# Optimization experiments

Measured on AMD Instinct MI355X. Metric: run time of the kernel, lower is better.

The kernel has to match this reference:

```python
import jax, jax.numpy as jnp
import numpy as np

T, D, H, V, Z = 32, 128, 256, 32000, 256


def _gru_cell(x, h, W_ih, W_hh, b_ih, b_hh):
    # PyTorch GRU cell, gate order r,z,n. x,h: [D,H]
    gi = x @ W_ih.T + b_ih
    gh = h @ W_hh.T + b_hh
    i_r, i_z, i_n = jnp.split(gi, 3, axis=-1)
    h_r, h_z, h_n = jnp.split(gh, 3, axis=-1)
    r = jax.nn.sigmoid(i_r + h_r)
    z = jax.nn.sigmoid(i_z + h_z)
    n = jnp.tanh(i_n + r * h_n)
    return (1.0 - z) * n + z * h


def _tree_rnn(nodes, edges, h0, emb, pc, ps):
    # nodes/edges: [T,D]; h0: [D,H]. Child vs sibling GRU chosen per-node by edges.
    def step(h, te):
        tok, e = te
        x = emb[tok]                       # [D,H]
        hc = _gru_cell(x, h, *pc)
        hs = _gru_cell(x, h, *ps)
        hn = jnp.where(e[:, None], hc, hs)  # branch-aware state update
        return hn, hn                       # seq_len=1, L=1 => output == new state
    h_final, outs = jax.lax.scan(step, h0, (nodes, edges))
    return outs, h_final                    # outs: [T,D,H]


def setup_inputs() -> dict:
    key = jax.random.key(0)
    ks = iter(jax.random.split(key, 48))
    s = 0.05
    def gru():
        return (jax.random.normal(next(ks), (3 * H, H), jnp.float32) * s,
                jax.random.normal(next(ks), (3 * H, H), jnp.float32) * s,
                jnp.zeros((3 * H,), jnp.float32),
                jnp.zeros((3 * H,), jnp.float32))
    inp = {}
    inp['nodes'] = jax.random.randint(next(ks), (T, D), 0, V, dtype=jnp.int32)
    inp['edges'] = jax.random.bernoulli(next(ks), 0.5, (T, D))
    inp['emb'] = jax.random.normal(next(ks), (V, H), jnp.float32) * s
    (inp['enc_c_Wih'], inp['enc_c_Whh'], inp['enc_c_bih'], inp['enc_c_bhh']) = gru()
    (inp['enc_s_Wih'], inp['enc_s_Whh'], inp['enc_s_bih'], inp['enc_s_bhh']) = gru()
    (inp['dec_c_Wih'], inp['dec_c_Whh'], inp['dec_c_bih'], inp['dec_c_bhh']) = gru()
    (inp['dec_s_Wih'], inp['dec_s_Whh'], inp['dec_s_bih'], inp['dec_s_bhh']) = gru()
    inp['W_mean'] = jax.random.normal(next(ks), (Z, H), jnp.float32) * s
    inp['b_mean'] = jnp.zeros((Z,), jnp.float32)
    inp['W_logv'] = jax.random.normal(next(ks), (Z, H), jnp.float32) * s
    inp['b_logv'] = jnp.zeros((Z,), jnp.float32)
    inp['W_l2h'] = jax.random.normal(next(ks), (H, Z), jnp.float32) * s
    inp['b_l2h'] = jnp.zeros((H,), jnp.float32)
    inp['W_out'] = jax.random.normal(next(ks), (V, H), jnp.float32) * s
    inp['b_out'] = jnp.zeros((V,), jnp.float32)
    inp['enc_init'] = jax.random.normal(next(ks), (D, H), jnp.float32) * 0.001
    inp['eps'] = jax.random.normal(next(ks), (D, Z), jnp.float32)
    return inp


def reference(nodes, edges, emb,
              enc_c_Wih, enc_c_Whh, enc_c_bih, enc_c_bhh,
              enc_s_Wih, enc_s_Whh, enc_s_bih, enc_s_bhh,
              dec_c_Wih, dec_c_Whh, dec_c_bih, dec_c_bhh,
              dec_s_Wih, dec_s_Whh, dec_s_bih, dec_s_bhh,
              W_mean, b_mean, W_logv, b_logv, W_l2h, b_l2h,
              W_out, b_out, enc_init, eps):
    pc_e = (enc_c_Wih, enc_c_Whh, enc_c_bih, enc_c_bhh)
    ps_e = (enc_s_Wih, enc_s_Whh, enc_s_bih, enc_s_bhh)
    pc_d = (dec_c_Wih, dec_c_Whh, dec_c_bih, dec_c_bhh)
    ps_d = (dec_s_Wih, dec_s_Whh, dec_s_bih, dec_s_bhh)

    _, hid = _tree_rnn(nodes, edges, enc_init, emb, pc_e, ps_e)  # [D,H]
    mean = hid @ W_mean.T + b_mean                               # [D,Z]
    logv = hid @ W_logv.T + b_logv
    z = eps * jnp.exp(0.5 * logv) + mean                          # reparameterize
    h0 = z @ W_l2h.T + b_l2h                                      # [D,H]
    outs, _ = _tree_rnn(nodes, edges, h0, emb, pc_d, ps_d)        # [T,D,H]
    logits = outs @ W_out.T + b_out                               # [T,D,V]
    logp = jax.nn.log_softmax(logits, axis=-1)
    return logp, mean, logv, z
```

## Files before the change

kernel.cpp:

```cpp
#include <hip/hip_runtime.h>
#include <hip/hip_bf16.h>

#define TT 32
#define DD 128
#define HH 256
#define VV 32000
#define ZZ 256
#define NTL 50
#define NBLK 16
#define GHLP 100

typedef __attribute__((ext_vector_type(8))) short bf16x8;
typedef __attribute__((ext_vector_type(4))) float f32x4;
typedef __attribute__((ext_vector_type(8))) _Float16 f16x8;

static __device__ inline unsigned short f2bf(float x) {
    __hip_bfloat16 h = __float2bfloat16(x);
    return *(unsigned short*)&h;
}

static __device__ inline unsigned long long pack4h(_Float16 a, _Float16 b,
                                                   _Float16 c, _Float16 d) {
    union { _Float16 h[4]; unsigned long long u; } x;
    x.h[0] = a; x.h[1] = b; x.h[2] = c; x.h[3] = d;
    return x.u;
}

static __device__ inline void gload_lds16(const void* g, void* l) {
    __builtin_amdgcn_global_load_lds(
        (const __attribute__((address_space(1))) void*)g,
        (__attribute__((address_space(3))) void*)l, 16, 0, 0);
}

__global__ void edge_canon_k(const unsigned char* __restrict__ eb,
                             unsigned char* __restrict__ canon)
{
    __shared__ int flag;
    if (threadIdx.x == 0) flag = 0;
    __syncthreads();
    int acc = 0;
    for (int i = threadIdx.x; i < TT * DD; i += 256)
        if (i & 3) acc |= eb[i];
    if (acc) atomicOr(&flag, 1);
    __syncthreads();
    const bool is_i32 = (flag == 0);
    for (int i = threadIdx.x; i < TT * DD; i += 256)
        canon[i] = is_i32 ? eb[4 * (size_t)i] : eb[i];
}

__global__ __launch_bounds__(256) void pack_frag(
    const float* __restrict__ src, __hip_bfloat16* __restrict__ dst, int nchunks_total)
{
    int i = blockIdx.x * 256 + threadIdx.x;
    if (i >= nchunks_total) return;
    int lane = i & 63, ks = (i >> 6) & 7, j = i >> 9;
    int g = lane >> 4, c = lane & 15;
    const float* s = src + (size_t)(j * 16 + c) * HH + ks * 32 + g * 8;
    float4 v0 = *(const float4*)s;
    float4 v1 = *(const float4*)(s + 4);
    bf16x8 o;
    o[0] = (short)f2bf(v0.x); o[1] = (short)f2bf(v0.y);
    o[2] = (short)f2bf(v0.z); o[3] = (short)f2bf(v0.w);
    o[4] = (short)f2bf(v1.x); o[5] = (short)f2bf(v1.y);
    o[6] = (short)f2bf(v1.z); o[7] = (short)f2bf(v1.w);
    *(bf16x8*)(dst + (size_t)i * 8) = o;
}

__global__ __launch_bounds__(256) void pack_frag4(
    const float* __restrict__ s0, const float* __restrict__ s1,
    const float* __restrict__ s2, const float* __restrict__ s3,
    __hip_bfloat16* __restrict__ dst)
{
    int i = blockIdx.x * 256 + threadIdx.x;
    if (i >= 24576) return;
    int slot = blockIdx.y;
    const float* src = (slot == 0) ? s0 : (slot == 1) ? s1 : (slot == 2) ? s2 : s3;
    __hip_bfloat16* d = dst + (size_t)slot * 196608;
    int lane = i & 63, ks = (i >> 6) & 7, j = i >> 9;
    int g = lane >> 4, c = lane & 15;
    const float* s = src + (size_t)(j * 16 + c) * HH + ks * 32 + g * 8;
    float4 v0 = *(const float4*)s;
    float4 v1 = *(const float4*)(s + 4);
    bf16x8 o;
    o[0] = (short)f2bf(v0.x); o[1] = (short)f2bf(v0.y);
    o[2] = (short)f2bf(v0.z); o[3] = (short)f2bf(v0.w);
    o[4] = (short)f2bf(v1.x); o[5] = (short)f2bf(v1.y);
    o[6] = (short)f2bf(v1.z); o[7] = (short)f2bf(v1.w);
    *(bf16x8*)(d + (size_t)i * 8) = o;
}

__global__ __launch_bounds__(256) void pack_wrnn4(
    const float* __restrict__ s0, const float* __restrict__ s1,
    const float* __restrict__ s2, const float* __restrict__ s3,
    _Float16* __restrict__ dst)
{
    int i = blockIdx.x * 256 + threadIdx.x;
    if (i >= 24576) return;
    int slot = blockIdx.y;
    const float* src = (slot == 0) ? s0 : (slot == 1) ? s1 : (slot == 2) ? s2 : s3;
    _Float16* d = dst + (size_t)slot * 196608;
    int lane = i & 63;
    int t2 = i >> 6;
    int ks = t2 & 7;
    int t3 = t2 >> 3;
    int tt = t3 % 6;
    int j8 = t3 / 6;
    int g = lane >> 4, c = lane & 15;
    int jg2 = tt / 3, gt = tt % 3;
    int srow = gt * 256 + j8 * 32 + jg2 * 16 + c;
    int scol = ks * 32 + g * 8;
    const float* s = src + (size_t)srow * HH + scol;
    float4 v0 = *(const float4*)s;
    float4 v1 = *(const float4*)(s + 4);
    f16x8 o;
    o[0] = (_Float16)v0.x; o[1] = (_Float16)v0.y;
    o[2] = (_Float16)v0.z; o[3] = (_Float16)v0.w;
    o[4] = (_Float16)v1.x; o[5] = (_Float16)v1.y;
    o[6] = (_Float16)v1.z; o[7] = (_Float16)v1.w;
    *(f16x8*)(d + (size_t)i * 8) = o;
}

__global__ __launch_bounds__(256) void gather_pack(
    const int* __restrict__ nodes, const float* __restrict__ emb,
    __hip_bfloat16* __restrict__ dst)
{
    int i = blockIdx.x * 256 + threadIdx.x;
    int lane = i & 63, ks = (i >> 6) & 7, j = i >> 9;
    int g = lane >> 4, c = lane & 15;
    int row = j * 16 + c;
    int tok = nodes[row];
    const float* s = emb + (size_t)tok * HH + ks * 32 + g * 8;
    float4 v0 = *(const float4*)s;
    float4 v1 = *(const float4*)(s + 4);
    bf16x8 o;
    o[0] = (short)f2bf(v0.x); o[1] = (short)f2bf(v0.y);
    o[2] = (short)f2bf(v0.z); o[3] = (short)f2bf(v0.w);
    o[4] = (short)f2bf(v1.x); o[5] = (short)f2bf(v1.y);
    o[6] = (short)f2bf(v1.z); o[7] = (short)f2bf(v1.w);
    *(bf16x8*)(dst + (size_t)i * 8) = o;
}

__global__ __launch_bounds__(256) void pack_lat3(
    const float* __restrict__ s0, const float* __restrict__ s1,
    const float* __restrict__ s2, float* __restrict__ dst)
{
    int i = blockIdx.x * 256 + threadIdx.x;
    int slot = blockIdx.y;
    const float* src = (slot == 0) ? s0 : (slot == 1) ? s1 : s2;
    float* d = dst + (size_t)slot * 65536;
    int j = i & 255, k = i >> 8;
    d[(size_t)k * 256 + j] = src[(size_t)j * 256 + k];
}

template<int MT, bool WRITE_C, bool HAS_BIAS, bool LSE_PARTIAL, bool LSE_SUB>
__global__ __launch_bounds__(256, 2) void gemm_rs(
    const __hip_bfloat16* __restrict__ A,
    const __hip_bfloat16* __restrict__ B,
    int ldc, int nchunks, int ntiles,
    const float* __restrict__ bias,
    const float* __restrict__ lse,
    float* __restrict__ C,
    float* __restrict__ pm, float* __restrict__ ps)
{
    __shared__ float lds_st[WRITE_C ? (4 * 16 * 68) : 1];

    const int tid  = threadIdx.x;
    const int w    = tid >> 6;
    const int lane = tid & 63;
    const int g    = lane >> 4;
    const int c    = lane & 15;
    const int m0   = blockIdx.x * (64 * MT);
    const int n0   = blockIdx.y * (nchunks * 64);
    const int jb0  = n0 >> 4;

    bf16x8 a[MT][8];
#pragma unroll
    for (int mt = 0; mt < MT; ++mt) {
        const int row16 = m0 + mt * 64 + w * 16;
        const __hip_bfloat16* ap = A + (((size_t)(row16 >> 4) * 8) * 64 + lane) * 8;
#pragma unroll
        for (int ks = 0; ks < 8; ++ks) a[mt][ks] = *(const bf16x8*)(ap + ks * 512);
    }

    float mrun[MT][4], srun[MT][4];
#pragma unroll
    for (int mt = 0; mt < MT; ++mt)
#pragma unroll
        for (int r = 0; r < 4; ++r) { mrun[mt][r] = -3.0e38f; srun[mt][r] = 0.f; }

    float lsev[MT][4];
    if (LSE_SUB) {
#pragma unroll
        for (int mt = 0; mt < MT; ++mt)
#pragma unroll
            for (int r = 0; r < 4; ++r)
                lsev[mt][r] = lse[m0 + mt * 64 + w * 16 + 4 * g + r];
    }

    for (int nc = 0; nc < nchunks; ++nc) {
        const int nb = n0 + nc * 64;
        const __hip_bfloat16* bp = B + (((size_t)(jb0 + nc * 4) * 8) * 64 + lane) * 8;

        f32x4 acc[MT][4];
#pragma unroll
        for (int mt = 0; mt < MT; ++mt)
#pragma unroll
            for (int nf = 0; nf < 4; ++nf) acc[mt][nf] = (f32x4){0.f, 0.f, 0.f, 0.f};

#pragma unroll
        for (int ks = 0; ks < 8; ++ks) {
            bf16x8 b0 = *(const bf16x8*)(bp + (0 * 8 + ks) * 512);
            bf16x8 b1 = *(const bf16x8*)(bp + (1 * 8 + ks) * 512);
            bf16x8 b2 = *(const bf16x8*)(bp + (2 * 8 + ks) * 512);
            bf16x8 b3 = *(const bf16x8*)(bp + (3 * 8 + ks) * 512);
#pragma unroll
            for (int mt = 0; mt < MT; ++mt) {
                acc[mt][0] = __builtin_amdgcn_mfma_f32_16x16x32_bf16(a[mt][ks], b0, acc[mt][0], 0, 0, 0);
                acc[mt][1] = __builtin_amdgcn_mfma_f32_16x16x32_bf16(a[mt][ks], b1, acc[mt][1], 0, 0, 0);
                acc[mt][2] = __builtin_amdgcn_mfma_f32_16x16x32_bf16(a[mt][ks], b2, acc[mt][2], 0, 0, 0);
                acc[mt][3] = __builtin_amdgcn_mfma_f32_16x16x32_bf16(a[mt][ks], b3, acc[mt][3], 0, 0, 0);
            }
        }

        float bv[4] = {0.f, 0.f, 0.f, 0.f};
        if (HAS_BIAS) {
#pragma unroll
            for (int nf = 0; nf < 4; ++nf) bv[nf] = bias[nb + nf * 16 + c];
        }

        if (LSE_PARTIAL) {
#pragma unroll
            for (int mt = 0; mt < MT; ++mt)
#pragma unroll
                for (int r = 0; r < 4; ++r) {
                    float l0 = acc[mt][0][r] + bv[0];
                    float l1 = acc[mt][1][r] + bv[1];
                    float l2 = acc[mt][2][r] + bv[2];
                    float l3 = acc[mt][3][r] + bv[3];
                    float mc = fmaxf(fmaxf(l0, l1), fmaxf(l2, l3));
                    float mn = fmaxf(mrun[mt][r], mc);
                    srun[mt][r] = srun[mt][r] * __expf(mrun[mt][r] - mn)
                            + __expf(l0 - mn) + __expf(l1 - mn)
                            + __expf(l2 - mn) + __expf(l3 - mn);
                    mrun[mt][r] = mn;
                }
        }

        if (WRITE_C) {
            const int base = w * (16 * 68);
#pragma unroll
            for (int mt = 0; mt < MT; ++mt) {
                const int row16 = m0 + mt * 64 + w * 16;
#pragma unroll
                for (int nf = 0; nf < 4; ++nf)
#pragma unroll
                    for (int r = 0; r < 4; ++r) {
                        float v = acc[mt][nf][r] + bv[nf];
                        if (LSE_SUB) v -= lsev[mt][r];
                        lds_st[base + (4 * g + r) * 68 + nf * 16 + c] = v;
                    }
#pragma unroll
                for (int i = 0; i < 4; ++i) {
                    int lr = i * 4 + g;
                    float4 v = *(const float4*)&lds_st[base + lr * 68 + c * 4];
                    *(float4*)(C + (size_t)(row16 + lr) * ldc + nb + c * 4) = v;
                }
            }
        }
    }

    if (LSE_PARTIAL) {
#pragma unroll
        for (int mt = 0; mt < MT; ++mt)
#pragma unroll
            for (int r = 0; r < 4; ++r) {
                float m = mrun[mt][r], s = srun[mt][r];
#pragma unroll
                for (int mk = 1; mk <= 8; mk <<= 1) {
                    float m2 = __shfl_xor(m, mk);
                    float s2 = __shfl_xor(s, mk);
                    float mn = fmaxf(m, m2);
                    s = s * __expf(m - mn) + s2 * __expf(m2 - mn);
                    m = mn;
                }
                if (c == 0) {
                    int row = m0 + mt * 64 + w * 16 + 4 * g + r;
                    pm[(size_t)row * ntiles + blockIdx.y] = m;
                    ps[(size_t)row * ntiles + blockIdx.y] = s;
                }
            }
    }
}

template<bool WRITE_C, bool HAS_BIAS, bool LSE_PARTIAL, bool LSE_SUB>
__global__ __launch_bounds__(256, 2) void gemm_ls(
    const __hip_bfloat16* __restrict__ A,
    const __hip_bfloat16* __restrict__ B,
    int ldc, int nchunks, int ntiles,
    const float* __restrict__ bias,
    const float* __restrict__ lse,
    float* __restrict__ C,
    float* __restrict__ pm, float* __restrict__ ps)
{
    __shared__ __align__(16) char ldsB[2][32768];
    __shared__ float lds_st[WRITE_C ? (4 * 16 * 68) : 1];

    const int tid  = threadIdx.x;
    const int w    = tid >> 6;
    const int lane = tid & 63;
    const int g    = lane >> 4;
    const int c    = lane & 15;
    const int m0   = blockIdx.x * 128;
    const int n0   = blockIdx.y * (nchunks * 64);
    const int jb0  = n0 >> 4;

    bf16x8 a[2][8];
#pragma unroll
    for (int mt = 0; mt < 2; ++mt) {
        const int row16 = m0 + mt * 64 + w * 16;
        const __hip_bfloat16* ap = A + (((size_t)(row16 >> 4) * 8) * 64 + lane) * 8;
#pragma unroll
        for (int ks = 0; ks < 8; ++ks) a[mt][ks] = *(const bf16x8*)(ap + ks * 512);
    }

    float mrun[2][4], srun[2][4];
#pragma unroll
    for (int mt = 0; mt < 2; ++mt)
#pragma unroll
        for (int r = 0; r < 4; ++r) { mrun[mt][r] = -3.0e38f; srun[mt][r] = 0.f; }

    float lsev[2][4];
    if (LSE_SUB) {
#pragma unroll
        for (int mt = 0; mt < 2; ++mt)
#pragma unroll
            for (int r = 0; r < 4; ++r)
                lsev[mt][r] = lse[m0 + mt * 64 + w * 16 + 4 * g + r];
    }

    const char* Bbase = (const char*)B;
#define STAGE_TILE(bbuf, nc_)                                                     \
    {                                                                             \
        const char* src = Bbase + ((size_t)(jb0 + (nc_) * 4) * 8 * 64) * 16;      \
        _Pragma("unroll")                                                         \
        for (int i_ = 0; i_ < 8; ++i_) {                                          \
            int seg = w * 8 + i_;                                                 \
            gload_lds16(src + (size_t)seg * 1024 + lane * 16,                     \
                        &ldsB[bbuf][seg * 1024]);                                 \
        }                                                                         \
    }

    int buf = 0;
    STAGE_TILE(0, 0);
    __syncthreads();

    for (int nc = 0; nc < nchunks; ++nc) {
        if (nc + 1 < nchunks) STAGE_TILE(buf ^ 1, nc + 1);

        const int nb = n0 + nc * 64;
        f32x4 acc[2][4];
#pragma unroll
        for (int mt = 0; mt < 2; ++mt)
#pragma unroll
            for (int nf = 0; nf < 4; ++nf) acc[mt][nf] = (f32x4){0.f, 0.f, 0.f, 0.f};

#pragma unroll
        for (int ks = 0; ks < 8; ++ks) {
            bf16x8 b0 = *(const bf16x8*)&ldsB[buf][((0 * 8 + ks) * 64 + lane) * 16];
            bf16x8 b1 = *(const bf16x8*)&ldsB[buf][((1 * 8 + ks) * 64 + lane) * 16];
            bf16x8 b2 = *(const bf16x8*)&ldsB[buf][((2 * 8 + ks) * 64 + lane) * 16];
            bf16x8 b3 = *(const bf16x8*)&ldsB[buf][((3 * 8 + ks) * 64 + lane) * 16];
#pragma unroll
            for (int mt = 0; mt < 2; ++mt) {
                acc[mt][0] = __builtin_amdgcn_mfma_f32_16x16x32_bf16(a[mt][ks], b0, acc[mt][0], 0, 0, 0);
                acc[mt][1] = __builtin_amdgcn_mfma_f32_16x16x32_bf16(a[mt][ks], b1, acc[mt][1], 0, 0, 0);
                acc[mt][2] = __builtin_amdgcn_mfma_f32_16x16x32_bf16(a[mt][ks], b2, acc[mt][2], 0, 0, 0);
                acc[mt][3] = __builtin_amdgcn_mfma_f32_16x16x32_bf16(a[mt][ks], b3, acc[mt][3], 0, 0, 0);
            }
        }

        float bv[4] = {0.f, 0.f, 0.f, 0.f};
        if (HAS_BIAS) {
#pragma unroll
            for (int nf = 0; nf < 4; ++nf) bv[nf] = bias[nb + nf * 16 + c];
        }

        if (LSE_PARTIAL) {
#pragma unroll
            for (int mt = 0; mt < 2; ++mt)
#pragma unroll
                for (int r = 0; r < 4; ++r) {
                    float l0 = acc[mt][0][r] + bv[0];
                    float l1 = acc[mt][1][r] + bv[1];
                    float l2 = acc[mt][2][r] + bv[2];
                    float l3 = acc[mt][3][r] + bv[3];
                    float mc = fmaxf(fmaxf(l0, l1), fmaxf(l2, l3));
                    float mn = fmaxf(mrun[mt][r], mc);
                    srun[mt][r] = srun[mt][r] * __expf(mrun[mt][r] - mn)
                            + __expf(l0 - mn) + __expf(l1 - mn)
                            + __expf(l2 - mn) + __expf(l3 - mn);
                    mrun[mt][r] = mn;
                }
        }

        if (WRITE_C) {
            const int base = w * (16 * 68);
#pragma unroll
            for (int mt = 0; mt < 2; ++mt) {
                const int row16 = m0 + mt * 64 + w * 16;
#pragma unroll
                for (int nf = 0; nf < 4; ++nf)
#pragma unroll
                    for (int r = 0; r < 4; ++r) {
                        float v = acc[mt][nf][r] + bv[nf];
                        if (LSE_SUB) v -= lsev[mt][r];
                        lds_st[base + (4 * g + r) * 68 + nf * 16 + c] = v;
                    }
#pragma unroll
                for (int i = 0; i < 4; ++i) {
                    int lr = i * 4 + g;
                    float4 v = *(const float4*)&lds_st[base + lr * 68 + c * 4];
                    *(float4*)(C + (size_t)(row16 + lr) * ldc + nb + c * 4) = v;
                }
            }
        }

        __syncthreads();
        buf ^= 1;
    }
#undef STAGE_TILE

    if (LSE_PARTIAL) {
#pragma unroll
        for (int mt = 0; mt < 2; ++mt)
#pragma unroll
            for (int r = 0; r < 4; ++r) {
                float m = mrun[mt][r], s = srun[mt][r];
#pragma unroll
                for (int mk = 1; mk <= 8; mk <<= 1) {
                    float m2 = __shfl_xor(m, mk);
                    float s2 = __shfl_xor(s, mk);
                    float mn = fmaxf(m, m2);
                    s = s * __expf(m - mn) + s2 * __expf(m2 - mn);
                    m = mn;
                }
                if (c == 0) {
                    int row = m0 + mt * 64 + w * 16 + 4 * g + r;
                    pm[(size_t)row * ntiles + blockIdx.y] = m;
                    ps[(size_t)row * ntiles + blockIdx.y] = s;
                }
            }
    }
}

__global__ __launch_bounds__(512) void rnn_fused6(
    const unsigned char* __restrict__ ecan,
    const float* __restrict__ gi,
    const _Float16* __restrict__ Wr,
    const float* __restrict__ ecbih, const float* __restrict__ ecbhh,
    const float* __restrict__ esbih, const float* __restrict__ esbhh,
    const float* __restrict__ dcbih, const float* __restrict__ dcbhh,
    const float* __restrict__ dsbih, const float* __restrict__ dsbhh,
    const float* __restrict__ WmT, const float* __restrict__ WlT,
    const float* __restrict__ WhT,
    const float* __restrict__ b_mean, const float* __restrict__ b_logv,
    const float* __restrict__ b_l2h,
    const float* __restrict__ enc_init, const float* __restrict__ eps,
    float* __restrict__ out_mean, float* __restrict__ out_logv,
    float* __restrict__ out_z,
    __hip_bfloat16* __restrict__ outs_pk,
    _Float16* __restrict__ xh,
    int* __restrict__ flags)
{
    __shared__ _Float16 wlds[6 * 8 * 64 * 8];
    __shared__ _Float16 hpk[64 * 64 * 8];
    __shared__ _Float16 ghl[DD * GHLP];
    __shared__ float    bsum[4 * 256];
    __shared__ unsigned char ecan_l[TT * DD];

    const int v   = blockIdx.x & 1;
    const int j8  = blockIdx.x >> 1;
    const int tid = threadIdx.x;
    const int w    = tid >> 6;
    const int lane = tid & 63;
    const int g    = lane >> 4;
    const int c    = lane & 15;
    const int dq   = w & 3;
    const int jg2  = w >> 2;

    for (int u = tid; u < TT * DD; u += 512) ecan_l[u] = ecan[u];

    for (int u = tid; u < 4096; u += 512) {
        int chunk = u >> 6, ln = u & 63;
        int dt = chunk >> 3, ks = chunk & 7, lg = ln >> 4, lc = ln & 15;
        const float* s = enc_init + (size_t)(dt * 16 + lc) * HH + ks * 32 + lg * 8;
        float4 v0 = *(const float4*)s;
        float4 v1 = *(const float4*)(s + 4);
        f16x8 o;
        o[0] = (_Float16)v0.x; o[1] = (_Float16)v0.y;
        o[2] = (_Float16)v0.z; o[3] = (_Float16)v0.w;
        o[4] = (_Float16)v1.x; o[5] = (_Float16)v1.y;
        o[6] = (_Float16)v1.z; o[7] = (_Float16)v1.w;
        *(f16x8*)&hpk[(size_t)u * 8] = o;
    }
    __syncthreads();

    int bi = 0;

    for (int p = 0; p < 2; ++p) {
        {
            const _Float16* wsrc = Wr + ((size_t)(p * 2 + v) * 8 + j8) * (3072 * 8);
            for (int idx = tid; idx < 3072; idx += 512)
                *(f16x8*)&wlds[(size_t)idx * 8] = *(const f16x8*)(wsrc + (size_t)idx * 8);
        }
        {
            const float* bih = p ? (v ? dsbih : dcbih) : (v ? esbih : ecbih);
            const float* bhh = p ? (v ? dsbhh : dcbhh) : (v ? esbhh : ecbhh);
            if (tid < 256) {
                bsum[tid]       = bih[tid]       + bhh[tid];
                bsum[256 + tid] = bih[256 + tid] + bhh[256 + tid];
                bsum[512 + tid] = bih[512 + tid];
                bsum[768 + tid] = bhh[512 + tid];
            }
        }
        __syncthreads();

        for (int st = 0; st < TT; ++st) {
            f32x4 gpr0[3], gpr1[3];
            bool sel0, sel1;
            {
                const int u0 = tid, u1 = tid + 512;
                const int d0 = u0 >> 3, d1 = u1 >> 3;
                const int jgA = j8 * 32 + (u0 & 7) * 4;
                const int jgB = j8 * 32 + (u1 & 7) * 4;
                sel0 = (ecan_l[st * DD + d0] != 0) == (v == 0);
                sel1 = (ecan_l[st * DD + d1] != 0) == (v == 0);
                if (sel0) {
                    const float* gp = gi + (size_t)(st * DD + d0) * 3072 + p * 1536 + v * 768 + jgA;
                    gpr0[0] = *(const f32x4*)gp;
                    gpr0[1] = *(const f32x4*)(gp + 256);
                    gpr0[2] = *(const f32x4*)(gp + 512);
                }
                if (sel1) {
                    const float* gp = gi + (size_t)(st * DD + d1) * 3072 + p * 1536 + v * 768 + jgB;
                    gpr1[0] = *(const f32x4*)gp;
                    gpr1[1] = *(const f32x4*)(gp + 256);
                    gpr1[2] = *(const f32x4*)(gp + 512);
                }
            }

            f32x4 acc[2][3];
#pragma unroll
            for (int a = 0; a < 2; ++a)
#pragma unroll
                for (int b = 0; b < 3; ++b) acc[a][b] = (f32x4){0.f, 0.f, 0.f, 0.f};
#pragma unroll
            for (int ks = 0; ks < 8; ++ks) {
                f16x8 a0 = *(const f16x8*)&hpk[(((dq * 2 + 0) * 8 + ks) * 64 + lane) * 8];
                f16x8 a1 = *(const f16x8*)&hpk[(((dq * 2 + 1) * 8 + ks) * 64 + lane) * 8];
#pragma unroll
                for (int gt = 0; gt < 3; ++gt) {
                    f16x8 bf = *(const f16x8*)&wlds[(((jg2 * 3 + gt) * 8 + ks) * 64 + lane) * 8];
                    acc[0][gt] = __builtin_amdgcn_mfma_f32_16x16x32_f16(a0, bf, acc[0][gt], 0, 0, 0);
                    acc[1][gt] = __builtin_amdgcn_mfma_f32_16x16x32_f16(a1, bf, acc[1][gt], 0, 0, 0);
                }
            }

#pragma unroll
            for (int dti = 0; dti < 2; ++dti) {
                const int dt = dq * 2 + dti;
#pragma unroll
                for (int gt = 0; gt < 3; ++gt)
#pragma unroll
                    for (int rr = 0; rr < 4; ++rr)
                        ghl[(dt * 16 + 4 * g + rr) * GHLP + gt * 32 + jg2 * 16 + c] =
                            (_Float16)acc[dti][gt][rr];
            }
            __syncthreads();

            _Float16* xcur = xh + (size_t)bi * (DD * HH);
#pragma unroll
            for (int uu = 0; uu < 2; ++uu) {
                const bool sel = uu ? sel1 : sel0;
                if (!sel) continue;
                const int u = tid + uu * 512;
                const int d = u >> 3, jq = u & 7;
                const int jl = jq * 4;
                const int jg_ = j8 * 32 + jl;
                const f32x4* gpr = uu ? gpr1 : gpr0;

                f32x4 br  = *(const f32x4*)&bsum[jg_];
                f32x4 bz  = *(const f32x4*)&bsum[256 + jg_];
                f32x4 bni = *(const f32x4*)&bsum[512 + jg_];
                f32x4 bnh = *(const f32x4*)&bsum[768 + jg_];
                const _Float16* gd = &ghl[d * GHLP];
                const int dt = d >> 4, lc = d & 15, ks = jg_ >> 5, lg = (jg_ >> 3) & 3;
                const int ch = ((dt * 8 + ks) * 64 + lg * 16 + lc);
                const _Float16* hop = &hpk[(size_t)ch * 8 + (jg_ & 7)];

                _Float16 hn[4];
                unsigned short ob[4];
#pragma unroll
                for (int m = 0; m < 4; ++m) {
                    float ghr = (float)gd[jl + m];
                    float ghz = (float)gd[32 + jl + m];
                    float ghn = (float)gd[64 + jl + m];
                    float rg = 1.f / (1.f + __expf(-(gpr[0][m] + br[m] + ghr)));
                    float zg = 1.f / (1.f + __expf(-(gpr[1][m] + bz[m] + ghz)));
                    float nn = tanhf(gpr[2][m] + bni[m] + rg * (ghn + bnh[m]));
                    float hv = (1.f - zg) * nn + zg * (float)hop[m];
                    hn[m] = (_Float16)hv;
                    ob[m] = f2bf(hv);
                }
                __hip_atomic_store((unsigned long long*)(xcur + (size_t)d * HH + jg_),
                                   pack4h(hn[0], hn[1], hn[2], hn[3]),
                                   __ATOMIC_RELAXED, __HIP_MEMORY_SCOPE_AGENT);
                if (p) {
                    union { unsigned short s[4]; unsigned long long u; } ou;
                    ou.s[0] = ob[0]; ou.s[1] = ob[1]; ou.s[2] = ob[2]; ou.s[3] = ob[3];
                    size_t och = ((size_t)(st * 8 + dt) * 8 + ks) * 64 + lg * 16 + lc;
                    *(unsigned long long*)((unsigned short*)outs_pk + och * 8 + (jg_ & 7)) = ou.u;
                }
            }
            __syncthreads();

            if (tid == 0)
                __hip_atomic_store(&flags[blockIdx.x], bi + 1,
                                   __ATOMIC_RELAXED, __HIP_MEMORY_SCOPE_AGENT);
            if (tid < 64) {
                for (;;) {
                    int f = (tid < NBLK)
                          ? __hip_atomic_load(&flags[tid], __ATOMIC_RELAXED, __HIP_MEMORY_SCOPE_AGENT)
                          : 0x7fffffff;
                    if (__all(f >= bi + 1)) break;
                    __builtin_amdgcn_s_sleep(1);
                }
            }
            __syncthreads();

            {
                const _Float16* xr = xh + (size_t)bi * (DD * HH);
                f16x8 tv[8];
#pragma unroll
                for (int i = 0; i < 8; ++i) {
                    int u = tid + i * 512;
                    int chunk = u >> 6, ln = u & 63;
                    int dt = chunk >> 3, ks = chunk & 7, lg = ln >> 4, lc = ln & 15;
                    tv[i] = *(const f16x8*)(xr + (size_t)(dt * 16 + lc) * HH + ks * 32 + lg * 8);
                }
#pragma unroll
                for (int i = 0; i < 8; ++i)
                    *(f16x8*)&hpk[(size_t)(tid + i * 512) * 8] = tv[i];
            }
            __syncthreads();
            ++bi;
        }

        if (p == 0) {
            float* hlin = (float*)ghl;
            const int d8 = tid >> 6;
            const int q  = tid & 63;
            const int dg = blockIdx.x * 8 + d8;
            for (int u = tid; u < 2048; u += 512) {
                int du = u >> 8, k = u & 255;
                int d = blockIdx.x * 8 + du;
                hlin[du * 256 + k] = (float)hpk[(((size_t)(d >> 4) * 8 + (k >> 5)) * 64
                                      + ((k >> 3) & 3) * 16 + (d & 15)) * 8 + (k & 7)];
            }
            __syncthreads();
            f32x4 mean4, logv4;
            {
                f32x4 sm = {0, 0, 0, 0}, sl = {0, 0, 0, 0};
                const float* hl = hlin + d8 * 256;
                for (int k = 0; k < HH; ++k) {
                    float hv = hl[k];
                    sm += hv * *(const f32x4*)(WmT + (size_t)k * 256 + q * 4);
                    sl += hv * *(const f32x4*)(WlT + (size_t)k * 256 + q * 4);
                }
                mean4 = sm + *(const f32x4*)(b_mean + q * 4);
                logv4 = sl + *(const f32x4*)(b_logv + q * 4);
                *(f32x4*)(out_mean + (size_t)dg * ZZ + q * 4) = mean4;
                *(f32x4*)(out_logv + (size_t)dg * ZZ + q * 4) = logv4;
            }
            __syncthreads();
            {
                f32x4 ep = *(const f32x4*)(eps + (size_t)dg * ZZ + q * 4);
                f32x4 zv;
#pragma unroll
                for (int m = 0; m < 4; ++m)
                    zv[m] = ep[m] * __expf(0.5f * logv4[m]) + mean4[m];
                *(f32x4*)(out_z + (size_t)dg * ZZ + q * 4) = zv;
                *(f32x4*)(hlin + d8 * 256 + q * 4) = zv;
            }
            __syncthreads();
            {
                f32x4 s = {0, 0, 0, 0};
                const float* zlp = hlin + d8 * 256;
                for (int k = 0; k < ZZ; ++k)
                    s += zlp[k] * *(const f32x4*)(WhT + (size_t)k * 256 + q * 4);
                f32x4 h0v = s + *(const f32x4*)(b_l2h + q * 4);
                __hip_atomic_store(
                    (unsigned long long*)(xh + (size_t)bi * (DD * HH) + (size_t)dg * HH + q * 4),
                    pack4h((_Float16)h0v[0], (_Float16)h0v[1],
                           (_Float16)h0v[2], (_Float16)h0v[3]),
                    __ATOMIC_RELAXED, __HIP_MEMORY_SCOPE_AGENT);
            }
            __syncthreads();
            if (tid == 0)
                __hip_atomic_store(&flags[blockIdx.x], bi + 1,
                                   __ATOMIC_RELAXED, __HIP_MEMORY_SCOPE_AGENT);
            if (tid < 64) {
                for (;;) {
                    int f = (tid < NBLK)
                          ? __hip_atomic_load(&flags[tid], __ATOMIC_RELAXED, __HIP_MEMORY_SCOPE_AGENT)
                          : 0x7fffffff;
                    if (__all(f >= bi + 1)) break;
                    __builtin_amdgcn_s_sleep(1);
                }
            }
            __syncthreads();
            {
                const _Float16* xr = xh + (size_t)bi * (DD * HH);
                f16x8 tv[8];
#pragma unroll
                for (int i = 0; i < 8; ++i) {
                    int u = tid + i * 512;
                    int chunk = u >> 6, ln = u & 63;
                    int dt = chunk >> 3, ks = chunk & 7, lg = ln >> 4, lc = ln & 15;
                    tv[i] = *(const f16x8*)(xr + (size_t)(dt * 16 + lc) * HH + ks * 32 + lg * 8);
                }
#pragma unroll
                for (int i = 0; i < 8; ++i)
                    *(f16x8*)&hpk[(size_t)(tid + i * 512) * 8] = tv[i];
            }
            __syncthreads();
            ++bi;
        }
    }
}

__global__ __launch_bounds__(64) void lse_reduce(
    const float* __restrict__ pm, const float* __restrict__ ps,
    float* __restrict__ lse, int nt)
{
    int row = blockIdx.x;
    int l = threadIdx.x;
    float m = (l < nt) ? pm[(size_t)row * nt + l] : -3.0e38f;
    float s = (l < nt) ? ps[(size_t)row * nt + l] : 0.f;
    for (int mk = 1; mk <= 32; mk <<= 1) {
        float m2 = __shfl_xor(m, mk);
        float s2 = __shfl_xor(s, mk);
        float mn = fmaxf(m, m2);
        s = s * __expf(m - mn) + s2 * __expf(m2 - mn);
        m = mn;
    }
    if (l == 0) lse[row] = m + logf(s);
}

extern "C" void kernel_launch(void* const* d_in, const int* in_sizes, int n_in,
                              void* d_out, int out_size, void* d_ws, size_t ws_size,
                              hipStream_t stream)
{
    const int*           nodes     = (const int*)d_in[0];
    const unsigned char* edges_raw = (const unsigned char*)d_in[1];
    const float* emb    = (const float*)d_in[2];
    const float* ecWih  = (const float*)d_in[3];
    const float* ecWhh  = (const float*)d_in[4];
    const float* ecbih  = (const float*)d_in[5];
    const float* ecbhh  = (const float*)d_in[6];
    const float* esWih  = (const float*)d_in[7];
    const float* esWhh  = (const float*)d_in[8];
    const float* esbih  = (const float*)d_in[9];
    const float* esbhh  = (const float*)d_in[10];
    const float* dcWih  = (const float*)d_in[11];
    const float* dcWhh  = (const float*)d_in[12];
    const float* dcbih  = (const float*)d_in[13];
    const float* dcbhh  = (const float*)d_in[14];
    const float* dsWih  = (const float*)d_in[15];
    const float* dsWhh  = (const float*)d_in[16];
    const float* dsbih  = (const float*)d_in[17];
    const float* dsbhh  = (const float*)d_in[18];
    const float* W_mean = (const float*)d_in[19];
    const float* b_mean = (const float*)d_in[20];
    const float* W_logv = (const float*)d_in[21];
    const float* b_logv = (const float*)d_in[22];
    const float* W_l2h  = (const float*)d_in[23];
    const float* b_l2h  = (const float*)d_in[24];
    const float* W_out  = (const float*)d_in[25];
    const float* b_out  = (const float*)d_in[26];
    const float* enc_init = (const float*)d_in[27];
    const float* eps    = (const float*)d_in[28];

    float* out      = (float*)d_out;
    float* out_mean = out + (size_t)TT * DD * VV;
    float* out_logv = out_mean + DD * ZZ;
    float* out_z    = out_logv + DD * ZZ;
    float* gi       = out;

    char* ws = (char*)d_ws;
    __hip_bfloat16* outs_pk = (__hip_bfloat16*)(ws + 0);
    __hip_bfloat16* Ap      = (__hip_bfloat16*)(ws + 2097152);
    __hip_bfloat16* Wp      = (__hip_bfloat16*)(ws + 4194304);
    __hip_bfloat16* Bp_all  = (__hip_bfloat16*)(ws + 20971520);
    _Float16*       Wr      = (_Float16*)(ws + 22544384);
    float*          WmT     = (float*)(ws + 24117248);
    float*          pm      = (float*)(ws + 24903680);
    float*          ps      = (float*)(ws + 25722880);
    float*          lse     = (float*)(ws + 26542080);
    unsigned char*  ecan    = (unsigned char*)(ws + 26558464);
    _Float16*       xh      = (_Float16*)(ws + 26562560);
    int*            flags   = (int*)(ws + 30822400);
    float*          WlT     = WmT + 65536;
    float*          WhT     = WmT + 131072;

    hipMemsetAsync(flags, 0, 64, stream);

    edge_canon_k<<<1, 256, 0, stream>>>(edges_raw, ecan);
    pack_frag<<<4000, 256, 0, stream>>>(W_out, Wp, 2000 * 8 * 64);
    pack_frag4<<<dim3(96, 4), 256, 0, stream>>>(ecWih, esWih, dcWih, dsWih, Bp_all);
    pack_wrnn4<<<dim3(96, 4), 256, 0, stream>>>(ecWhh, esWhh, dcWhh, dsWhh, Wr);
    pack_lat3<<<dim3(256, 3), 256, 0, stream>>>(W_mean, W_logv, W_l2h, WmT);
    gather_pack<<<512, 256, 0, stream>>>(nodes, emb, Ap);

    gemm_rs<2, true, false, false, false><<<dim3(32, 6), 256, 0, stream>>>(
        Ap, Bp_all, 3072, 8, 6, nullptr, nullptr, gi, nullptr, nullptr);

    rnn_fused6<<<NBLK, 512, 0, stream>>>(
        ecan, gi, Wr,
        ecbih, ecbhh, esbih, esbhh, dcbih, dcbhh, dsbih, dsbhh,
        WmT, WlT, WhT, b_mean, b_logv, b_l2h,
        enc_init, eps, out_mean, out_logv, out_z, outs_pk, xh, flags);

    gemm_ls<false, true, true, false><<<dim3(32, NTL), 256, 0, stream>>>(
        outs_pk, Wp, VV, 10, NTL, b_out, nullptr, nullptr, pm, ps);
    lse_reduce<<<4096, 64, 0, stream>>>(pm, ps, lse, NTL);
    gemm_ls<true, true, false, true><<<dim3(32, NTL), 256, 0, stream>>>(
        outs_pk, Wp, VV, 10, NTL, b_out, lse, out, nullptr, nullptr);
}
```

Measured before the change: 811.0 us.

## Overlap W_out packing with RNN kernel and single-buffer the write-out GEMM

The standalone W_out bf16 fragment-pack kernel is folded into the recurrent RNN kernel as extra blocks beyond the 16 RNN blocks. Those blocks pack W_out while the latency-bound RNN runs on only a few CUs, hiding the pack time. The final logits-writing GEMM now uses a single LDS buffer instead of double buffering. This frees shared memory for occupancy but exposes load latency because it syncs after each stage. One risk is that the RNN blocks may spin on flags and need co-residency, so the 2000 extra blocks could delay scheduling or contend with the RNN blocks.

```diff
diff --git a/kernel.cpp b/kernel.cpp
--- a/kernel.cpp
+++ b/kernel.cpp
@@ -8,6 +8,7 @@
 #define ZZ 256
 #define NTL 50
 #define NBLK 16
+#define NPACK 2000
 #define GHLP 100
 
 typedef __attribute__((ext_vector_type(8))) short bf16x8;
@@ -46,24 +47,6 @@
     const bool is_i32 = (flag == 0);
     for (int i = threadIdx.x; i < TT * DD; i += 256)
         canon[i] = is_i32 ? eb[4 * (size_t)i] : eb[i];
-}
-
-__global__ __launch_bounds__(256) void pack_frag(
-    const float* __restrict__ src, __hip_bfloat16* __restrict__ dst, int nchunks_total)
-{
-    int i = blockIdx.x * 256 + threadIdx.x;
-    if (i >= nchunks_total) return;
-    int lane = i & 63, ks = (i >> 6) & 7, j = i >> 9;
-    int g = lane >> 4, c = lane & 15;
-    const float* s = src + (size_t)(j * 16 + c) * HH + ks * 32 + g * 8;
-    float4 v0 = *(const float4*)s;
-    float4 v1 = *(const float4*)(s + 4);
-    bf16x8 o;
-    o[0] = (short)f2bf(v0.x); o[1] = (short)f2bf(v0.y);
-    o[2] = (short)f2bf(v0.z); o[3] = (short)f2bf(v0.w);
-    o[4] = (short)f2bf(v1.x); o[5] = (short)f2bf(v1.y);
-    o[6] = (short)f2bf(v1.z); o[7] = (short)f2bf(v1.w);
-    *(bf16x8*)(dst + (size_t)i * 8) = o;
 }
 
 __global__ __launch_bounds__(256) void pack_frag4(
@@ -292,7 +275,7 @@
     }
 }
 
-template<bool WRITE_C, bool HAS_BIAS, bool LSE_PARTIAL, bool LSE_SUB>
+template<bool DBUF, bool WRITE_C, bool HAS_BIAS, bool LSE_PARTIAL, bool LSE_SUB>
 __global__ __launch_bounds__(256, 2) void gemm_ls(
     const __hip_bfloat16* __restrict__ A,
     const __hip_bfloat16* __restrict__ B,
@@ -302,7 +285,7 @@
     float* __restrict__ C,
     float* __restrict__ pm, float* __restrict__ ps)
 {
-    __shared__ __align__(16) char ldsB[2][32768];
+    __shared__ __align__(16) char ldsB[DBUF ? 2 : 1][32768];
     __shared__ float lds_st[WRITE_C ? (4 * 16 * 68) : 1];
 
     const int tid  = threadIdx.x;
@@ -351,11 +334,18 @@
     }
 
     int buf = 0;
-    STAGE_TILE(0, 0);
-    __syncthreads();
+    if (DBUF) {
+        STAGE_TILE(0, 0);
+        __syncthreads();
+    }
 
     for (int nc = 0; nc < nchunks; ++nc) {
-        if (nc + 1 < nchunks) STAGE_TILE(buf ^ 1, nc + 1);
+        if (DBUF) {
+            if (nc + 1 < nchunks) STAGE_TILE(buf ^ 1, nc + 1);
+        } else {
+            STAGE_TILE(0, nc);
+            __syncthreads();
+        }
 
         const int nb = n0 + nc * 64;
         f32x4 acc[2][4];
@@ -426,7 +416,7 @@
         }
 
         __syncthreads();
-        buf ^= 1;
+        if (DBUF) buf ^= 1;
     }
 #undef STAGE_TILE
 
@@ -470,7 +460,8 @@
     float* __restrict__ out_z,
     __hip_bfloat16* __restrict__ outs_pk,
     _Float16* __restrict__ xh,
-    int* __restrict__ flags)
+    int* __restrict__ flags,
+    const float* __restrict__ W_out, __hip_bfloat16* __restrict__ Wp)
 {
     __shared__ _Float16 wlds[6 * 8 * 64 * 8];
     __shared__ _Float16 hpk[64 * 64 * 8];
@@ -478,9 +469,28 @@
     __shared__ float    bsum[4 * 256];
     __shared__ unsigned char ecan_l[TT * DD];
 
+    const int tid = threadIdx.x;
+
+    if (blockIdx.x >= NBLK) {
+        int i = (blockIdx.x - NBLK) * 512 + tid;
+        if (i < 2000 * 8 * 64) {
+            int lane = i & 63, ks = (i >> 6) & 7, j = i >> 9;
+            int g2 = lane >> 4, c2 = lane & 15;
+            const float* s = W_out + (size_t)(j * 16 + c2) * HH + ks * 32 + g2 * 8;
+            float4 v0 = *(const float4*)s;
+            float4 v1 = *(const float4*)(s + 4);
+            bf16x8 o;
+            o[0] = (short)f2bf(v0.x); o[1] = (short)f2bf(v0.y);
+            o[2] = (short)f2bf(v0.z); o[3] = (short)f2bf(v0.w);
+            o[4] = (short)f2bf(v1.x); o[5] = (short)f2bf(v1.y);
+            o[6] = (short)f2bf(v1.z); o[7] = (short)f2bf(v1.w);
+            *(bf16x8*)(Wp + (size_t)i * 8) = o;
+        }
+        return;
+    }
+
     const int v   = blockIdx.x & 1;
     const int j8  = blockIdx.x >> 1;
-    const int tid = threadIdx.x;
     const int w    = tid >> 6;
     const int lane = tid & 63;
     const int g    = lane >> 4;
@@ -816,7 +826,6 @@
     hipMemsetAsync(flags, 0, 64, stream);
 
     edge_canon_k<<<1, 256, 0, stream>>>(edges_raw, ecan);
-    pack_frag<<<4000, 256, 0, stream>>>(W_out, Wp, 2000 * 8 * 64);
     pack_frag4<<<dim3(96, 4), 256, 0, stream>>>(ecWih, esWih, dcWih, dsWih, Bp_all);
     pack_wrnn4<<<dim3(96, 4), 256, 0, stream>>>(ecWhh, esWhh, dcWhh, dsWhh, Wr);
     pack_lat3<<<dim3(256, 3), 256, 0, stream>>>(W_mean, W_logv, W_l2h, WmT);
@@ -825,15 +834,16 @@
     gemm_rs<2, true, false, false, false><<<dim3(32, 6), 256, 0, stream>>>(
         Ap, Bp_all, 3072, 8, 6, nullptr, nullptr, gi, nullptr, nullptr);
 
-    rnn_fused6<<<NBLK, 512, 0, stream>>>(
+    rnn_fused6<<<NBLK + NPACK, 512, 0, stream>>>(
         ecan, gi, Wr,
         ecbih, ecbhh, esbih, esbhh, dcbih, dcbhh, dsbih, dsbhh,
         WmT, WlT, WhT, b_mean, b_logv, b_l2h,
-        enc_init, eps, out_mean, out_logv, out_z, outs_pk, xh, flags);
-
-    gemm_ls<false, true, true, false><<<dim3(32, NTL), 256, 0, stream>>>(
+        enc_init, eps, out_mean, out_logv, out_z, outs_pk, xh, flags,
+        W_out, Wp);
+
+    gemm_ls<true, false, true, true, false><<<dim3(32, NTL), 256, 0, stream>>>(
         outs_pk, Wp, VV, 10, NTL, b_out, nullptr, nullptr, pm, ps);
     lse_reduce<<<4096, 64, 0, stream>>>(pm, ps, lse, NTL);
-    gemm_ls<true, true, false, true><<<dim3(32, NTL), 256, 0, stream>>>(
+    gemm_ls<false, true, true, false, true><<<dim3(32, NTL), 256, 0, stream>>>(
         outs_pk, Wp, VV, 10, NTL, b_out, lse, out, nullptr, nullptr);
 }
```

Result: faster. 759.7 us (-6.3%).
